# Kernel optimization log

Measured on AMD Instinct MI355X. Metric: run time of the kernel, lower is better.

## Reference

```python
import jax, jax.numpy as jnp
import numpy as np

M = 262144          # rows of A == prod(out_shape) == 512*512
N = 262144          # cols of A == prod(x.shape)
NNZ = 8388608       # 32 nonzeros per row on average
OUT_SHAPE = (512, 512)


def setup_inputs() -> dict:
    key = jax.random.key(0)
    k1, k2, k3, k4 = jax.random.split(key, 4)
    A_rows = jax.random.randint(k1, (NNZ,), 0, M, dtype=jnp.int32)
    A_cols = jax.random.randint(k2, (NNZ,), 0, N, dtype=jnp.int32)
    A_vals = jax.random.normal(k3, (NNZ,), dtype=jnp.float32)
    x = jax.random.normal(k4, OUT_SHAPE, dtype=jnp.float32)
    return {"x": x, "A_vals": A_vals, "A_rows": A_rows, "A_cols": A_cols}


def reference(x, A_vals, A_rows, A_cols):
    # x.reshape(A.shape[1], 1); torch.sparse.mm(A, x); reshape(out_shape)
    xf = x.reshape(-1)                                   # [N]
    contrib = A_vals * jnp.take(xf, A_cols)              # [NNZ] gather + multiply
    y = jax.ops.segment_sum(contrib, A_rows, num_segments=M)  # scatter-add over rows
    return y.reshape(OUT_SHAPE).astype(jnp.float32)
```

## Files before the change

### kernel.cpp

```cpp
#include <hip/hip_runtime.h>


#define BINS            64
#define ROW_SHIFT       12
#define ROWS_PER_BIN    4096
#define ENT             4096
#define SCATTER_THREADS 512
#define NWAVES          8
#define IPT             8
#define SLICES          8
#define ACCUM_THREADS   1024


__global__ __launch_bounds__(256) void zero_out_kernel(float* __restrict__ y, int n) {
    int i = blockIdx.x * blockDim.x + threadIdx.x;
    if (i < n) y[i] = 0.0f;
}

__global__ __launch_bounds__(256) void spmv_coo_scatter(
    const float* __restrict__ vals, const int* __restrict__ rows,
    const int* __restrict__ cols, const float* __restrict__ x,
    float* __restrict__ y, int nnz)
{
    int i = (blockIdx.x * blockDim.x + threadIdx.x) * 4;
    if (i + 3 < nnz) {
        float4 v = *reinterpret_cast<const float4*>(vals + i);
        int4   r = *reinterpret_cast<const int4*>(rows + i);
        int4   c = *reinterpret_cast<const int4*>(cols + i);
        atomicAdd(&y[r.x], v.x * x[c.x]);
        atomicAdd(&y[r.y], v.y * x[c.y]);
        atomicAdd(&y[r.z], v.z * x[c.z]);
        atomicAdd(&y[r.w], v.w * x[c.w]);
    } else {
        for (; i < nnz; ++i) atomicAdd(&y[rows[i]], vals[i] * x[cols[i]]);
    }
}


__global__ __launch_bounds__(64) void init_cursors(unsigned* __restrict__ gcur) {
    gcur[threadIdx.x] = 0u;
}

__global__ __launch_bounds__(SCATTER_THREADS, 8) void scatter4_kernel(
    const int*   __restrict__ rows, const int* __restrict__ cols,
    const float* __restrict__ vals, const float* __restrict__ x, int nnz,
    unsigned* __restrict__ gcur, unsigned cap,
    unsigned short* __restrict__ okeys, float* __restrict__ ocontrib)
{
    __shared__ unsigned cnt[NWAVES * BINS];
    __shared__ unsigned cur2[NWAVES * BINS];
    __shared__ int      dstb[BINS];
    __shared__ unsigned total_s;
    __shared__ unsigned short skey[ENT];
    __shared__ float          sval[ENT];
    __shared__ unsigned char  sbin[ENT];

    const int t   = threadIdx.x;
    const int wid = t >> 6;
    for (int i = t; i < NWAVES * BINS; i += SCATTER_THREADS) cnt[i] = 0u;
    __syncthreads();

    const int seg = blockIdx.x * ENT;
    int   rr[IPT];
    float ff[IPT];

    #pragma unroll
    for (int ch = 0; ch < IPT / 4; ++ch) {
        int base = seg + ch * (SCATTER_THREADS * 4) + t * 4;
        if (base + 3 < nnz) {
            int4   r4 = *reinterpret_cast<const int4*>(rows + base);
            int4   c4 = *reinterpret_cast<const int4*>(cols + base);
            float4 v4 = *reinterpret_cast<const float4*>(vals + base);
            rr[ch*4+0] = r4.x; ff[ch*4+0] = v4.x * x[c4.x];
            rr[ch*4+1] = r4.y; ff[ch*4+1] = v4.y * x[c4.y];
            rr[ch*4+2] = r4.z; ff[ch*4+2] = v4.z * x[c4.z];
            rr[ch*4+3] = r4.w; ff[ch*4+3] = v4.w * x[c4.w];
        } else {
            #pragma unroll
            for (int j = 0; j < 4; ++j) {
                int idx = base + j;
                if (idx < nnz) { rr[ch*4+j] = rows[idx]; ff[ch*4+j] = vals[idx] * x[cols[idx]]; }
                else           { rr[ch*4+j] = -1; ff[ch*4+j] = 0.0f; }
            }
        }
    }
    #pragma unroll
    for (int j = 0; j < IPT; ++j)
        if (rr[j] >= 0) atomicAdd(&cnt[wid * BINS + (rr[j] >> ROW_SHIFT)], 1u);
    __syncthreads();

    if (t < BINS) {
        unsigned tot = 0;
        #pragma unroll
        for (int w = 0; w < NWAVES; ++w) tot += cnt[w * BINS + t];
        unsigned resv = atomicAdd(&gcur[t], tot);
        unsigned inc = tot;
        #pragma unroll
        for (int off = 1; off < 64; off <<= 1) {
            unsigned v = __shfl_up(inc, off, 64);
            if (t >= off) inc += v;
        }
        unsigned lst = inc - tot;
        dstb[t] = (int)resv - (int)lst;
        if (t == 63) total_s = inc;
        unsigned o = lst;
        #pragma unroll
        for (int w = 0; w < NWAVES; ++w) { cur2[w * BINS + t] = o; o += cnt[w * BINS + t]; }
    }
    __syncthreads();

    #pragma unroll
    for (int j = 0; j < IPT; ++j) {
        if (rr[j] >= 0) {
            int b = rr[j] >> ROW_SHIFT;
            unsigned p = atomicAdd(&cur2[wid * BINS + b], 1u);
            skey[p] = (unsigned short)(rr[j] & (ROWS_PER_BIN - 1));
            sval[p] = ff[j];
            sbin[p] = (unsigned char)b;
        }
    }
    __syncthreads();

    const unsigned total = total_s;
    for (unsigned i = t; i < total; i += SCATTER_THREADS) {
        int b = sbin[i];
        unsigned off = (unsigned)(dstb[b] + (int)i);
        if (off < cap) {
            size_t dst = (size_t)b * cap + off;
            okeys[dst]    = skey[i];
            ocontrib[dst] = sval[i];
        }
    }
}

__global__ __launch_bounds__(ACCUM_THREADS, 8) void accum4_kernel(
    const unsigned short* __restrict__ okeys, const float* __restrict__ ocontrib,
    const unsigned* __restrict__ gcur, unsigned cap,
    float* __restrict__ partials)
{
    __shared__ float acc[ROWS_PER_BIN];
    const int t   = threadIdx.x;
    const int bin = blockIdx.x / SLICES;
    const int sl  = blockIdx.x % SLICES;

    *reinterpret_cast<float4*>(&acc[t * 4]) = make_float4(0.f, 0.f, 0.f, 0.f);
    __syncthreads();

    unsigned count = gcur[bin];
    if (count > cap) count = cap;
    unsigned chunk = (count + SLICES - 1) / SLICES;
    chunk = (chunk + 3u) & ~3u;
    unsigned lo = (unsigned)sl * chunk;
    unsigned hi = lo + chunk; if (hi > count) hi = count;

    const unsigned short* k = okeys    + (size_t)bin * cap;
    const float*          c = ocontrib + (size_t)bin * cap;

    unsigned i = lo + (unsigned)t * 4u;
    for (; i + 3u < hi; i += (unsigned)ACCUM_THREADS * 4u) {
        ushort4 k4 = *reinterpret_cast<const ushort4*>(k + i);
        float4  c4 = *reinterpret_cast<const float4*>(c + i);
        atomicAdd(&acc[k4.x], c4.x);
        atomicAdd(&acc[k4.y], c4.y);
        atomicAdd(&acc[k4.z], c4.z);
        atomicAdd(&acc[k4.w], c4.w);
    }
    for (; i < hi; ++i) atomicAdd(&acc[k[i]], c[i]);
    __syncthreads();

    float* p = partials + (size_t)blockIdx.x * ROWS_PER_BIN;
    *reinterpret_cast<float4*>(p + t * 4) = *reinterpret_cast<const float4*>(&acc[t * 4]);
}

__global__ __launch_bounds__(256) void reduce4_kernel(
    const float* __restrict__ partials, float* __restrict__ y, int out_size)
{
    int r = (blockIdx.x * 256 + threadIdx.x) * 4;
    if (r >= out_size) return;
    int bin = r >> ROW_SHIFT, local = r & (ROWS_PER_BIN - 1);
    const float* p = partials + ((size_t)bin * SLICES) * ROWS_PER_BIN + local;
    float4 s = make_float4(0.f, 0.f, 0.f, 0.f);
    #pragma unroll
    for (int j = 0; j < SLICES; ++j) {
        float4 v = *reinterpret_cast<const float4*>(p + (size_t)j * ROWS_PER_BIN);
        s.x += v.x; s.y += v.y; s.z += v.z; s.w += v.w;
    }
    *reinterpret_cast<float4*>(y + r) = s;
}

extern "C" void kernel_launch(void* const* d_in, const int* in_sizes, int n_in,
                              void* d_out, int out_size, void* d_ws, size_t ws_size,
                              hipStream_t stream) {
    const float* x    = (const float*)d_in[0];
    const float* vals = (const float*)d_in[1];
    const int*   rows = (const int*)d_in[2];
    const int*   cols = (const int*)d_in[3];
    float* y = (float*)d_out;

    const int nnz = in_sizes[1];
    const int nb  = (nnz + ENT - 1) / ENT;
    unsigned cap  = (unsigned)(nnz / BINS) + 8192u;
    cap = (cap + 3u) & ~3u;

    auto align256 = [](size_t v) { return (v + 255) & ~(size_t)255; };
    size_t off_contrib  = 0;
    size_t off_keys     = align256(off_contrib + (size_t)BINS * cap * 4);
    size_t off_partials = align256(off_keys + (size_t)BINS * cap * 2);
    size_t off_gcur     = align256(off_partials + (size_t)BINS * SLICES * ROWS_PER_BIN * 4);
    size_t need         = align256(off_gcur + (size_t)BINS * 4);

    const bool ok = (out_size <= BINS * ROWS_PER_BIN) && (out_size % 4 == 0) &&
                    (need <= ws_size) && (nnz > 0);

    if (!ok) {
        zero_out_kernel<<<(out_size + 255) / 256, 256, 0, stream>>>(y, out_size);
        spmv_coo_scatter<<<(nnz + 1023) / 1024, 256, 0, stream>>>(vals, rows, cols, x, y, nnz);
        return;
    }

    char* w = (char*)d_ws;
    float*          ocontrib = (float*)(w + off_contrib);
    unsigned short* okeys    = (unsigned short*)(w + off_keys);
    float*          partials = (float*)(w + off_partials);
    unsigned*       gcur     = (unsigned*)(w + off_gcur);

    init_cursors<<<1, BINS, 0, stream>>>(gcur);
    scatter4_kernel<<<nb, SCATTER_THREADS, 0, stream>>>(rows, cols, vals, x, nnz,
                                                        gcur, cap, okeys, ocontrib);
    accum4_kernel<<<BINS * SLICES, ACCUM_THREADS, 0, stream>>>(okeys, ocontrib, gcur, cap, partials);
    reduce4_kernel<<<(out_size / 4 + 255) / 256, 256, 0, stream>>>(partials, y, out_size);
}
```

Measured before the change: 235.9 us.

## Pack bin key and contribution into 64-bit entries and retune accumulation slicing

The scatter stage now stores each nonzero as one packed 64-bit word (float contribution in the high half, bin and local row in the low half) in a single buffer. Shared staging and global writes use that one array instead of separate key, value and bin arrays. The accumulate stage reads two packed entries per 16-byte load and uses 16 slices with 512 threads instead of 8 slices with 1024. This cuts separate narrow stores and gives more parallel accumulation blocks, at the cost of 8 rather than 6 bytes per entry and twice as many partials for the reduce to read.

```diff
diff --git a/kernel.cpp b/kernel.cpp
--- a/kernel.cpp
+++ b/kernel.cpp
@@ -8,8 +8,8 @@
 #define SCATTER_THREADS 512
 #define NWAVES          8
 #define IPT             8
-#define SLICES          8
-#define ACCUM_THREADS   1024
+#define SLICES          16
+#define ACCUM_THREADS   512
 
 
 __global__ __launch_bounds__(256) void zero_out_kernel(float* __restrict__ y, int n) {
@@ -41,19 +41,22 @@
     gcur[threadIdx.x] = 0u;
 }
 
-__global__ __launch_bounds__(SCATTER_THREADS, 8) void scatter4_kernel(
+static __device__ __forceinline__ unsigned long long pack_entry(int row, float f) {
+    unsigned meta = ((unsigned)(row >> ROW_SHIFT) << 16) | (unsigned)(row & (ROWS_PER_BIN - 1));
+    return ((unsigned long long)__float_as_uint(f) << 32) | (unsigned long long)meta;
+}
+
+__global__ __launch_bounds__(SCATTER_THREADS, 8) void scatter5_kernel(
     const int*   __restrict__ rows, const int* __restrict__ cols,
     const float* __restrict__ vals, const float* __restrict__ x, int nnz,
     unsigned* __restrict__ gcur, unsigned cap,
-    unsigned short* __restrict__ okeys, float* __restrict__ ocontrib)
+    unsigned long long* __restrict__ obuf)
 {
     __shared__ unsigned cnt[NWAVES * BINS];
     __shared__ unsigned cur2[NWAVES * BINS];
     __shared__ int      dstb[BINS];
     __shared__ unsigned total_s;
-    __shared__ unsigned short skey[ENT];
-    __shared__ float          sval[ENT];
-    __shared__ unsigned char  sbin[ENT];
+    __shared__ unsigned long long sent[ENT];
 
     const int t   = threadIdx.x;
     const int wid = t >> 6;
@@ -114,27 +117,22 @@
         if (rr[j] >= 0) {
             int b = rr[j] >> ROW_SHIFT;
             unsigned p = atomicAdd(&cur2[wid * BINS + b], 1u);
-            skey[p] = (unsigned short)(rr[j] & (ROWS_PER_BIN - 1));
-            sval[p] = ff[j];
-            sbin[p] = (unsigned char)b;
+            sent[p] = pack_entry(rr[j], ff[j]);
         }
     }
     __syncthreads();
 
     const unsigned total = total_s;
     for (unsigned i = t; i < total; i += SCATTER_THREADS) {
-        int b = sbin[i];
+        unsigned long long e = sent[i];
+        unsigned b = ((unsigned)e >> 16) & 63u;
         unsigned off = (unsigned)(dstb[b] + (int)i);
-        if (off < cap) {
-            size_t dst = (size_t)b * cap + off;
-            okeys[dst]    = skey[i];
-            ocontrib[dst] = sval[i];
-        }
-    }
-}
-
-__global__ __launch_bounds__(ACCUM_THREADS, 8) void accum4_kernel(
-    const unsigned short* __restrict__ okeys, const float* __restrict__ ocontrib,
+        if (off < cap) obuf[(size_t)b * cap + off] = e;
+    }
+}
+
+__global__ __launch_bounds__(ACCUM_THREADS, 8) void accum5_kernel(
+    const unsigned long long* __restrict__ obuf,
     const unsigned* __restrict__ gcur, unsigned cap,
     float* __restrict__ partials)
 {
@@ -143,36 +141,43 @@
     const int bin = blockIdx.x / SLICES;
     const int sl  = blockIdx.x % SLICES;
 
-    *reinterpret_cast<float4*>(&acc[t * 4]) = make_float4(0.f, 0.f, 0.f, 0.f);
+    #pragma unroll
+    for (int i = 0; i < ROWS_PER_BIN / (ACCUM_THREADS * 4); ++i) {
+        int l = (i * ACCUM_THREADS + t) * 4;
+        *reinterpret_cast<float4*>(&acc[l]) = make_float4(0.f, 0.f, 0.f, 0.f);
+    }
     __syncthreads();
 
     unsigned count = gcur[bin];
     if (count > cap) count = cap;
     unsigned chunk = (count + SLICES - 1) / SLICES;
-    chunk = (chunk + 3u) & ~3u;
+    chunk = (chunk + 1u) & ~1u;
     unsigned lo = (unsigned)sl * chunk;
     unsigned hi = lo + chunk; if (hi > count) hi = count;
 
-    const unsigned short* k = okeys    + (size_t)bin * cap;
-    const float*          c = ocontrib + (size_t)bin * cap;
-
-    unsigned i = lo + (unsigned)t * 4u;
-    for (; i + 3u < hi; i += (unsigned)ACCUM_THREADS * 4u) {
-        ushort4 k4 = *reinterpret_cast<const ushort4*>(k + i);
-        float4  c4 = *reinterpret_cast<const float4*>(c + i);
-        atomicAdd(&acc[k4.x], c4.x);
-        atomicAdd(&acc[k4.y], c4.y);
-        atomicAdd(&acc[k4.z], c4.z);
-        atomicAdd(&acc[k4.w], c4.w);
-    }
-    for (; i < hi; ++i) atomicAdd(&acc[k[i]], c[i]);
+    const unsigned long long* e = obuf + (size_t)bin * cap;
+
+    unsigned i = lo + (unsigned)t * 2u;
+    for (; i + 1u < hi; i += (unsigned)ACCUM_THREADS * 2u) {
+        uint4 q = *reinterpret_cast<const uint4*>(e + i);
+        atomicAdd(&acc[q.x & 0xFFFFu], __uint_as_float(q.y));
+        atomicAdd(&acc[q.z & 0xFFFFu], __uint_as_float(q.w));
+    }
+    if (i < hi) {
+        unsigned long long q = e[i];
+        atomicAdd(&acc[(unsigned)q & 0xFFFFu], __uint_as_float((unsigned)(q >> 32)));
+    }
     __syncthreads();
 
     float* p = partials + (size_t)blockIdx.x * ROWS_PER_BIN;
-    *reinterpret_cast<float4*>(p + t * 4) = *reinterpret_cast<const float4*>(&acc[t * 4]);
-}
-
-__global__ __launch_bounds__(256) void reduce4_kernel(
+    #pragma unroll
+    for (int j = 0; j < ROWS_PER_BIN / (ACCUM_THREADS * 4); ++j) {
+        int l = (j * ACCUM_THREADS + t) * 4;
+        *reinterpret_cast<float4*>(p + l) = *reinterpret_cast<const float4*>(&acc[l]);
+    }
+}
+
+__global__ __launch_bounds__(256) void reduce5_kernel(
     const float* __restrict__ partials, float* __restrict__ y, int out_size)
 {
     int r = (blockIdx.x * 256 + threadIdx.x) * 4;
@@ -203,9 +208,8 @@
     cap = (cap + 3u) & ~3u;
 
     auto align256 = [](size_t v) { return (v + 255) & ~(size_t)255; };
-    size_t off_contrib  = 0;
-    size_t off_keys     = align256(off_contrib + (size_t)BINS * cap * 4);
-    size_t off_partials = align256(off_keys + (size_t)BINS * cap * 2);
+    size_t off_obuf     = 0;
+    size_t off_partials = align256(off_obuf + (size_t)BINS * cap * 8);
     size_t off_gcur     = align256(off_partials + (size_t)BINS * SLICES * ROWS_PER_BIN * 4);
     size_t need         = align256(off_gcur + (size_t)BINS * 4);
 
@@ -219,14 +223,13 @@
     }
 
     char* w = (char*)d_ws;
-    float*          ocontrib = (float*)(w + off_contrib);
-    unsigned short* okeys    = (unsigned short*)(w + off_keys);
-    float*          partials = (float*)(w + off_partials);
-    unsigned*       gcur     = (unsigned*)(w + off_gcur);
+    unsigned long long* obuf     = (unsigned long long*)(w + off_obuf);
+    float*              partials = (float*)(w + off_partials);
+    unsigned*           gcur     = (unsigned*)(w + off_gcur);
 
     init_cursors<<<1, BINS, 0, stream>>>(gcur);
-    scatter4_kernel<<<nb, SCATTER_THREADS, 0, stream>>>(rows, cols, vals, x, nnz,
-                                                        gcur, cap, okeys, ocontrib);
-    accum4_kernel<<<BINS * SLICES, ACCUM_THREADS, 0, stream>>>(okeys, ocontrib, gcur, cap, partials);
-    reduce4_kernel<<<(out_size / 4 + 255) / 256, 256, 0, stream>>>(partials, y, out_size);
-}
+    scatter5_kernel<<<nb, SCATTER_THREADS, 0, stream>>>(rows, cols, vals, x, nnz,
+                                                        gcur, cap, obuf);
+    accum5_kernel<<<BINS * SLICES, ACCUM_THREADS, 0, stream>>>(obuf, gcur, cap, partials);
+    reduce5_kernel<<<(out_size / 4 + 255) / 256, 256, 0, stream>>>(partials, y, out_size);
+}
```

Measured after the change: 246.9 us. 1.05x slower.
